# Kernel tuning notes

Measured on AMD Instinct MI355X. Metric: run time of the kernel, lower is better.

The kernel has to match this reference:

```python
import jax, jax.numpy as jnp
import numpy as np

EMBED_DIM = 1024
HEADS = 16
HEAD_DIM = EMBED_DIM // HEADS


def setup_inputs() -> dict:
    key = jax.random.key(0)
    ks = jax.random.split(key, 5)
    B, N, C = 2, 2048, EMBED_DIM
    scale = 1.0 / np.sqrt(C)
    x = jax.random.normal(ks[0], (B, N, C), dtype=jnp.float32)
    W_qkv = jax.random.normal(ks[1], (C, 3 * C), dtype=jnp.float32) * scale
    b_qkv = jax.random.normal(ks[2], (3 * C,), dtype=jnp.float32) * 0.01
    W_out = jax.random.normal(ks[3], (C, C), dtype=jnp.float32) * scale
    b_out = jax.random.normal(ks[4], (C,), dtype=jnp.float32) * 0.01
    return {"x": x, "W_qkv": W_qkv, "b_qkv": b_qkv, "W_out": W_out, "b_out": b_out}


def reference(x, W_qkv, b_qkv, W_out, b_out):
    B, N, C = x.shape
    qkv = x @ W_qkv + b_qkv                      # [B, N, 3C]
    qkv = qkv.reshape(B, N, 3, HEADS, HEAD_DIM)
    qkv = jnp.transpose(qkv, (2, 0, 3, 1, 4))    # [3, B, H, N, d]
    q, k, v = qkv[0], qkv[1], qkv[2]
    attn = jnp.einsum('bhnd,bhmd->bhnm', q, k) / np.sqrt(HEAD_DIM)
    attn = jax.nn.softmax(attn, axis=-1)
    out = jnp.einsum('bhnm,bhmd->bhnd', attn, v)  # [B, H, N, d]
    out = jnp.transpose(out, (0, 2, 1, 3)).reshape(B, N, C)
    return out @ W_out + b_out
```

## Files before the change

kernel.cpp:

```cpp
#include <hip/hip_runtime.h>
#include <stdint.h>

typedef __bf16 bf16_t;
typedef bf16_t bf16x8 __attribute__((ext_vector_type(8)));
typedef short short4v __attribute__((ext_vector_type(4)));
typedef float f32x4 __attribute__((ext_vector_type(4)));
typedef uint32_t u32x2 __attribute__((ext_vector_type(2)));

#define BATCH 2
#define SEQ 2048
#define CDIM 1024
#define NH 16
#define HD 64

__device__ __forceinline__ uint16_t f32_bf16(float f) {
    uint32_t u = __builtin_bit_cast(uint32_t, f);
    uint32_t r = u + 0x7fffu + ((u >> 16) & 1u);
    return (uint16_t)(r >> 16);
}

__device__ __forceinline__ uint32_t pack_bf16(float a, float b) {
    uint32_t ua = __builtin_bit_cast(uint32_t, a);
    uint32_t ub = __builtin_bit_cast(uint32_t, b);
    ua += 0x7fffu + ((ua >> 16) & 1u);
    ub += 0x7fffu + ((ub >> 16) & 1u);
    return (ua >> 16) | (ub & 0xffff0000u);
}

__device__ __forceinline__ bf16x8 ld8(const uint16_t* p) {
    return *reinterpret_cast<const bf16x8*>(p);
}

__device__ __forceinline__ void gld16(const uint16_t* g, uint16_t* l) {
    __builtin_amdgcn_global_load_lds(
        (__attribute__((address_space(1))) void*)(g),
        (__attribute__((address_space(3))) void*)(l), 16, 0, 0);
}

#define LDS_FENCE() asm volatile("s_waitcnt lgkmcnt(0)" ::: "memory")

__global__ __launch_bounds__(256) void cast_f32_bf16(
        const float* __restrict__ in, uint16_t* __restrict__ out, int n) {
    int i = (blockIdx.x * 256 + threadIdx.x) * 4;
    if (i < n) {
        float4 v = *(const float4*)(in + i);
        ushort4 o;
        o.x = f32_bf16(v.x);
        o.y = f32_bf16(v.y);
        o.z = f32_bf16(v.z);
        o.w = f32_bf16(v.w);
        *(ushort4*)(out + i) = o;
    }
}

__global__ __launch_bounds__(256) void transpose_cast(
        const float* __restrict__ in, uint16_t* __restrict__ out, int R, int Cc) {
    __shared__ float tile[32][33];
    int c0 = blockIdx.x * 32, r0 = blockIdx.y * 32;
    int tx = threadIdx.x, ty = threadIdx.y;
#pragma unroll
    for (int i = 0; i < 4; i++) {
        int r = ty + i * 8;
        tile[r][tx] = in[(size_t)(r0 + r) * Cc + c0 + tx];
    }
    __syncthreads();
#pragma unroll
    for (int i = 0; i < 4; i++) {
        int rr = ty + i * 8;
        out[(size_t)(c0 + rr) * R + r0 + tx] = f32_bf16(tile[tx][rr]);
    }
}

__global__ __launch_bounds__(256) void gemm128(
        const uint16_t* __restrict__ A, const uint16_t* __restrict__ Bt, int K,
        const float* __restrict__ bias, int mode,
        uint16_t* __restrict__ qw, uint16_t* __restrict__ kw, uint16_t* __restrict__ vt,
        float* __restrict__ out) {
    __shared__ uint16_t As[128 * 32];
    __shared__ uint16_t Bs[128 * 32];
    __shared__ uint16_t Ts[4][64 * 68];
    const int m0 = blockIdx.y * 128, n0 = blockIdx.x * 128;
    const int tid = threadIdx.x;
    const int w = tid >> 6, lane = tid & 63;
    const int quad = lane >> 4, l16 = lane & 15;
    const int wm = (w >> 1) * 64, wn = (w & 1) * 64;

    const int srow = lane >> 2;
    const int schunk = (lane & 3) ^ (srow & 3);
    const int seg0 = w * 2, seg1 = seg0 + 1;
    const uint16_t* a0 = A + (size_t)(m0 + seg0 * 16 + srow) * K + schunk * 8;
    const uint16_t* a1 = A + (size_t)(m0 + seg1 * 16 + srow) * K + schunk * 8;
    const uint16_t* b0 = Bt + (size_t)(n0 + seg0 * 16 + srow) * K + schunk * 8;
    const uint16_t* b1 = Bt + (size_t)(n0 + seg1 * 16 + srow) * K + schunk * 8;
    uint16_t* la0 = &As[seg0 * 512];
    uint16_t* la1 = &As[seg1 * 512];
    uint16_t* lb0 = &Bs[seg0 * 512];
    uint16_t* lb1 = &Bs[seg1 * 512];

    const int cslot = (quad ^ (l16 & 3)) * 8;

    f32x4 acc[4][4] = {};

    for (int k0 = 0; k0 < K; k0 += 32) {
        gld16(a0 + k0, la0);
        gld16(a1 + k0, la1);
        gld16(b0 + k0, lb0);
        gld16(b1 + k0, lb1);
        __syncthreads();
        bf16x8 af[4], bfr[4];
#pragma unroll
        for (int i = 0; i < 4; i++) af[i] = ld8(&As[(wm + i * 16 + l16) * 32 + cslot]);
#pragma unroll
        for (int i = 0; i < 4; i++) bfr[i] = ld8(&Bs[(wn + i * 16 + l16) * 32 + cslot]);
#pragma unroll
        for (int i = 0; i < 4; i++)
#pragma unroll
            for (int j = 0; j < 4; j++)
                acc[i][j] = __builtin_amdgcn_mfma_f32_16x16x32_bf16(af[i], bfr[j], acc[i][j], 0, 0, 0);
        __syncthreads();
    }

    const int nbase = n0 + wn;
    float bj[4];
#pragma unroll
    for (int j = 0; j < 4; j++) bj[j] = bias[nbase + j * 16 + l16];

    if (mode == 1) {
#pragma unroll
        for (int j = 0; j < 4; j++) {
#pragma unroll
            for (int i = 0; i < 4; i++)
#pragma unroll
                for (int r = 0; r < 4; r++) {
                    int m = m0 + wm + i * 16 + quad * 4 + r;
                    out[(size_t)m * CDIM + nbase + j * 16 + l16] = acc[i][j][r] + bj[j];
                }
        }
        return;
    }

    uint16_t* T = &Ts[w][0];
    const int gmb = m0 + wm;
    const int b = gmb >> 11, ns0 = gmb & 2047;

    if (nbase < 2048) {
#pragma unroll
        for (int i = 0; i < 4; i++)
#pragma unroll
            for (int j = 0; j < 4; j++)
#pragma unroll
                for (int r = 0; r < 4; r++)
                    T[(i * 16 + quad * 4 + r) * 68 + j * 16 + l16] = f32_bf16(acc[i][j][r] + bj[j]);
        LDS_FENCE();
        const int which = nbase >> 10, h = (nbase & 1023) >> 6;
        uint16_t* dst = ((which == 0) ? qw : kw) +
                        (((size_t)b * NH + h) * SEQ + ns0 + lane) * HD;
#pragma unroll
        for (int g = 0; g < 8; g++) {
            bf16x8 v = ld8(&T[lane * 68 + g * 8]);
            *(bf16x8*)(dst + g * 8) = v;
        }
    } else {
#pragma unroll
        for (int i = 0; i < 4; i++)
#pragma unroll
            for (int j = 0; j < 4; j++) {
                u32x2 pr;
                pr.x = pack_bf16(acc[i][j][0] + bj[j], acc[i][j][1] + bj[j]);
                pr.y = pack_bf16(acc[i][j][2] + bj[j], acc[i][j][3] + bj[j]);
                *(u32x2*)&T[(j * 16 + l16) * 68 + i * 16 + quad * 4] = pr;
            }
        LDS_FENCE();
        const int h = (nbase - 2048) >> 6;
        uint16_t* dst = vt + (((size_t)b * NH + h) * HD + lane) * SEQ + ns0;
#pragma unroll
        for (int g = 0; g < 16; g++) {
            u32x2 d2 = *(const u32x2*)&T[lane * 68 + g * 4];
            int npos = (g & 3) * 16 + (g >> 2) * 4;
            *(u32x2*)(dst + npos) = d2;
        }
    }
}

__global__ __launch_bounds__(256) void attn_kernel(
        const uint16_t* __restrict__ qg, const uint16_t* __restrict__ kg,
        const uint16_t* __restrict__ vt, uint16_t* __restrict__ og) {
    __shared__ uint16_t Ks[2][64 * 64];
    __shared__ uint16_t Vs[2][64 * 64];

    const int bh = blockIdx.x;
    const int qt = blockIdx.y;
    const int tid = threadIdx.x;
    const int w = tid >> 6, lane = tid & 63;
    const int quad = lane >> 4, l16 = lane & 15;
    const int qrow0 = qt * 64 + w * 16;
    const size_t base = (size_t)bh * SEQ * HD;

    bf16x8 qf[2];
#pragma unroll
    for (int ks = 0; ks < 2; ks++)
        qf[ks] = ld8(qg + base + (size_t)(qrow0 + l16) * HD + ks * 32 + quad * 8);

    const int srow = lane >> 3;
    const int schunk = (lane & 7) ^ srow;
    const int seg0 = w * 2, seg1 = seg0 + 1;
    const uint16_t* ksrc0 = kg + base + (size_t)(seg0 * 8 + srow) * HD + schunk * 8;
    const uint16_t* ksrc1 = kg + base + (size_t)(seg1 * 8 + srow) * HD + schunk * 8;
    const uint16_t* vsrc0 = vt + base + (size_t)(seg0 * 8 + srow) * SEQ + schunk * 8;
    const uint16_t* vsrc1 = vt + base + (size_t)(seg1 * 8 + srow) * SEQ + schunk * 8;
    const int soff0 = seg0 * 512, soff1 = seg1 * 512;

    f32x4 o_acc[4] = {};
    float l_run = 0.f;
    const float c = 0.18033688011f;

    gld16(ksrc0, &Ks[0][soff0]); gld16(ksrc1, &Ks[0][soff1]);
    gld16(vsrc0, &Vs[0][soff0]); gld16(vsrc1, &Vs[0][soff1]);
    ksrc0 += 64 * HD; ksrc1 += 64 * HD; vsrc0 += 64; vsrc1 += 64;

    for (int it = 0; it < SEQ / 64; ++it) {
        __syncthreads();
        if (it + 1 < SEQ / 64) {
            int pb = (it + 1) & 1;
            gld16(ksrc0, &Ks[pb][soff0]); gld16(ksrc1, &Ks[pb][soff1]);
            gld16(vsrc0, &Vs[pb][soff0]); gld16(vsrc1, &Vs[pb][soff1]);
            ksrc0 += 64 * HD; ksrc1 += 64 * HD; vsrc0 += 64; vsrc1 += 64;
        }
        const uint16_t* K_ = Ks[it & 1];
        const uint16_t* V_ = Vs[it & 1];

        f32x4 S[4] = {};
#pragma unroll
        for (int nf = 0; nf < 4; nf++) {
#pragma unroll
            for (int ks = 0; ks < 2; ks++) {
                bf16x8 kf = ld8(&K_[(nf * 16 + l16) * 64 + (((ks * 4 + quad) ^ (l16 & 7)) * 8)]);
                S[nf] = __builtin_amdgcn_mfma_f32_16x16x32_bf16(kf, qf[ks], S[nf], 0, 0, 0);
            }
        }

        float rs = 0.f;
        uint32_t pk[4][2];
#pragma unroll
        for (int nf = 0; nf < 4; nf++) {
            float p0 = __builtin_amdgcn_exp2f(fmaf(S[nf][0], c, -14.f));
            float p1 = __builtin_amdgcn_exp2f(fmaf(S[nf][1], c, -14.f));
            float p2 = __builtin_amdgcn_exp2f(fmaf(S[nf][2], c, -14.f));
            float p3 = __builtin_amdgcn_exp2f(fmaf(S[nf][3], c, -14.f));
            rs += (p0 + p1) + (p2 + p3);
            pk[nf][0] = pack_bf16(p0, p1);
            pk[nf][1] = pack_bf16(p2, p3);
        }
        l_run += rs;

#pragma unroll
        for (int mf = 0; mf < 4; mf++) {
            const int ro = (mf * 16 + l16) * 64;
            uint4 v0 = *(const uint4*)&V_[ro + (((quad * 2 + 0) ^ (l16 & 7)) * 8)];
            uint4 v1 = *(const uint4*)&V_[ro + (((quad * 2 + 1) ^ (l16 & 7)) * 8)];
            short4v vf[4];
            vf[0] = __builtin_bit_cast(short4v, (u32x2){v0.x, v0.y});
            vf[1] = __builtin_bit_cast(short4v, (u32x2){v0.z, v0.w});
            vf[2] = __builtin_bit_cast(short4v, (u32x2){v1.x, v1.y});
            vf[3] = __builtin_bit_cast(short4v, (u32x2){v1.z, v1.w});
#pragma unroll
            for (int kc = 0; kc < 4; kc++) {
                short4v pfrag = __builtin_bit_cast(short4v, (u32x2){pk[kc][0], pk[kc][1]});
                o_acc[mf] = __builtin_amdgcn_mfma_f32_16x16x16bf16_1k(vf[kc], pfrag, o_acc[mf], 0, 0, 0);
            }
        }
    }

    l_run += __shfl_xor(l_run, 16);
    l_run += __shfl_xor(l_run, 32);
    const int b = bh >> 4, h = bh & 15;
    const float inv = __builtin_amdgcn_rcpf(l_run);
    const int ns = qrow0 + l16;
    uint16_t* orow = og + (((size_t)b * SEQ + ns) * NH + h) * HD + quad * 4;
#pragma unroll
    for (int mf = 0; mf < 4; mf++) {
        ushort4 o;
        o.x = f32_bf16(o_acc[mf][0] * inv);
        o.y = f32_bf16(o_acc[mf][1] * inv);
        o.z = f32_bf16(o_acc[mf][2] * inv);
        o.w = f32_bf16(o_acc[mf][3] * inv);
        *(ushort4*)(orow + mf * 16) = o;
    }
}

extern "C" void kernel_launch(void* const* d_in, const int* in_sizes, int n_in,
                              void* d_out, int out_size, void* d_ws, size_t ws_size,
                              hipStream_t stream) {
    const float* x = (const float*)d_in[0];
    const float* Wqkv = (const float*)d_in[1];
    const float* bqkv = (const float*)d_in[2];
    const float* Wout = (const float*)d_in[3];
    const float* bout = (const float*)d_in[4];
    float* out = (float*)d_out;

    uint16_t* ws = (uint16_t*)d_ws;
    uint16_t* x_bf  = ws;
    uint16_t* wqkvT = x_bf + 4194304;
    uint16_t* woutT = wqkvT + 3145728;
    uint16_t* qw    = woutT + 1048576;
    uint16_t* kw    = qw + 4194304;
    uint16_t* vtw   = kw + 4194304;
    uint16_t* attn  = vtw + 4194304;

    cast_f32_bf16<<<4096, 256, 0, stream>>>(x, x_bf, 4194304);
    transpose_cast<<<dim3(96, 32), dim3(32, 8), 0, stream>>>(Wqkv, wqkvT, 1024, 3072);
    transpose_cast<<<dim3(32, 32), dim3(32, 8), 0, stream>>>(Wout, woutT, 1024, 1024);

    gemm128<<<dim3(24, 32), 256, 0, stream>>>(x_bf, wqkvT, 1024, bqkv, 0, qw, kw, vtw, nullptr);

    attn_kernel<<<dim3(32, 32), 256, 0, stream>>>(qw, kw, vtw, attn);

    gemm128<<<dim3(8, 32), 256, 0, stream>>>(attn, woutT, 1024, bout, 1, nullptr, nullptr, nullptr, out);
}
```

Before: 219.1 us.

## Prescale Q by softmax constant, compute row sums via MFMA, use native bf16 casts

Folds the softmax log2e/sqrt(d) scale into Q during the QKV projection epilogue so the attention loop feeds scores straight into exp2. Row sums of P are accumulated with an MFMA against a ones fragment instead of VALU adds and cross-lane shuffles. Float-to-bf16 conversion uses native casts, which may map to hardware convert instructions. The fixed -14 exponent offset is removed, which risks overflow for large scores, and the extra MFMAs add matrix-core work.

Result: faster. 210.5 us (-3.9%).

```diff
diff --git a/kernel.cpp b/kernel.cpp
--- a/kernel.cpp
+++ b/kernel.cpp
@@ -3,6 +3,7 @@
 
 typedef __bf16 bf16_t;
 typedef bf16_t bf16x8 __attribute__((ext_vector_type(8)));
+typedef bf16_t bf16x2v __attribute__((ext_vector_type(2)));
 typedef short short4v __attribute__((ext_vector_type(4)));
 typedef float f32x4 __attribute__((ext_vector_type(4)));
 typedef uint32_t u32x2 __attribute__((ext_vector_type(2)));
@@ -13,18 +14,18 @@
 #define NH 16
 #define HD 64
 
+#define QSCALE 0.18033688011f
+
 __device__ __forceinline__ uint16_t f32_bf16(float f) {
-    uint32_t u = __builtin_bit_cast(uint32_t, f);
-    uint32_t r = u + 0x7fffu + ((u >> 16) & 1u);
-    return (uint16_t)(r >> 16);
+    __bf16 h = (__bf16)f;
+    return __builtin_bit_cast(uint16_t, h);
 }
 
 __device__ __forceinline__ uint32_t pack_bf16(float a, float b) {
-    uint32_t ua = __builtin_bit_cast(uint32_t, a);
-    uint32_t ub = __builtin_bit_cast(uint32_t, b);
-    ua += 0x7fffu + ((ua >> 16) & 1u);
-    ub += 0x7fffu + ((ub >> 16) & 1u);
-    return (ua >> 16) | (ub & 0xffff0000u);
+    bf16x2v t;
+    t.x = (__bf16)a;
+    t.y = (__bf16)b;
+    return __builtin_bit_cast(uint32_t, t);
 }
 
 __device__ __forceinline__ bf16x8 ld8(const uint16_t* p) {
@@ -144,15 +145,17 @@
     const int b = gmb >> 11, ns0 = gmb & 2047;
 
     if (nbase < 2048) {
+        const int which = nbase >> 10, h = (nbase & 1023) >> 6;
+        const float sc = (which == 0) ? QSCALE : 1.0f;
 #pragma unroll
         for (int i = 0; i < 4; i++)
 #pragma unroll
             for (int j = 0; j < 4; j++)
 #pragma unroll
                 for (int r = 0; r < 4; r++)
-                    T[(i * 16 + quad * 4 + r) * 68 + j * 16 + l16] = f32_bf16(acc[i][j][r] + bj[j]);
+                    T[(i * 16 + quad * 4 + r) * 68 + j * 16 + l16] =
+                        f32_bf16((acc[i][j][r] + bj[j]) * sc);
         LDS_FENCE();
-        const int which = nbase >> 10, h = (nbase & 1023) >> 6;
         uint16_t* dst = ((which == 0) ? qw : kw) +
                         (((size_t)b * NH + h) * SEQ + ns0 + lane) * HD;
 #pragma unroll
@@ -211,8 +214,8 @@
     const int soff0 = seg0 * 512, soff1 = seg1 * 512;
 
     f32x4 o_acc[4] = {};
-    float l_run = 0.f;
-    const float c = 0.18033688011f;
+    f32x4 l_acc = {};
+    const short4v ones = { (short)0x3F80, (short)0x3F80, (short)0x3F80, (short)0x3F80 };
 
     gld16(ksrc0, &Ks[0][soff0]); gld16(ksrc1, &Ks[0][soff1]);
     gld16(vsrc0, &Vs[0][soff0]); gld16(vsrc1, &Vs[0][soff1]);
@@ -239,19 +242,22 @@
             }
         }
 
-        float rs = 0.f;
         uint32_t pk[4][2];
 #pragma unroll
         for (int nf = 0; nf < 4; nf++) {
-            float p0 = __builtin_amdgcn_exp2f(fmaf(S[nf][0], c, -14.f));
-            float p1 = __builtin_amdgcn_exp2f(fmaf(S[nf][1], c, -14.f));
-            float p2 = __builtin_amdgcn_exp2f(fmaf(S[nf][2], c, -14.f));
-            float p3 = __builtin_amdgcn_exp2f(fmaf(S[nf][3], c, -14.f));
-            rs += (p0 + p1) + (p2 + p3);
+            float p0 = __builtin_amdgcn_exp2f(S[nf][0]);
+            float p1 = __builtin_amdgcn_exp2f(S[nf][1]);
+            float p2 = __builtin_amdgcn_exp2f(S[nf][2]);
+            float p3 = __builtin_amdgcn_exp2f(S[nf][3]);
             pk[nf][0] = pack_bf16(p0, p1);
             pk[nf][1] = pack_bf16(p2, p3);
         }
-        l_run += rs;
+
+#pragma unroll
+        for (int kc = 0; kc < 4; kc++) {
+            short4v pfrag = __builtin_bit_cast(short4v, (u32x2){pk[kc][0], pk[kc][1]});
+            l_acc = __builtin_amdgcn_mfma_f32_16x16x16bf16_1k(ones, pfrag, l_acc, 0, 0, 0);
+        }
 
 #pragma unroll
         for (int mf = 0; mf < 4; mf++) {
@@ -271,10 +277,8 @@
         }
     }
 
-    l_run += __shfl_xor(l_run, 16);
-    l_run += __shfl_xor(l_run, 32);
     const int b = bh >> 4, h = bh & 15;
-    const float inv = __builtin_amdgcn_rcpf(l_run);
+    const float inv = __builtin_amdgcn_rcpf(l_acc[0]);
     const int ns = qrow0 + l16;
     uint16_t* orow = og + (((size_t)b * SEQ + ns) * NH + h) * HD + quad * 4;
 #pragma unroll
```
